# Kernel optimization log

Hardware: AMD Instinct MI355X
Metric: run time of the kernel (lower is better)

Reference implementation:

```python
import jax, jax.numpy as jnp
import numpy as np

N_PATCHES = 14
HIDDEN_D = 768
N_HEADS = 12
D_HEAD = HIDDEN_D // N_HEADS
OUT_D = 1000
IMG = 224
C = 3
PS = IMG // N_PATCHES  # 16
SEQ = N_PATCHES * N_PATCHES + 1  # 197
INPUT_D = C * PS * PS  # 768
EPS = 1e-5


def positional_embeddings(s, d):
    i = jnp.arange(s, dtype=jnp.float32)[:, None]
    j = jnp.arange(d, dtype=jnp.float32)[None, :]
    even = jnp.sin(i / jnp.power(10000.0, j / d))
    odd = jnp.cos(i / jnp.power(10000.0, (j - 1.0) / d))
    return jnp.where(jnp.arange(d)[None, :] % 2 == 0, even, odd)


def layernorm_2d(x, g, b):
    # torch nn.LayerNorm((S, D)): normalize over last two dims jointly, biased var
    mu = jnp.mean(x, axis=(-2, -1), keepdims=True)
    var = jnp.var(x, axis=(-2, -1), keepdims=True)
    return (x - mu) * jax.lax.rsqrt(var + EPS) * g + b


def setup_inputs() -> dict:
    key = jax.random.key(0)
    ks = jax.random.split(key, 16)
    s = 0.02
    return {
        "images": jax.random.normal(ks[0], (64, C, IMG, IMG), jnp.float32),
        "W_map": jax.random.normal(ks[1], (INPUT_D, HIDDEN_D), jnp.float32) * s,
        "b_map": jnp.zeros((HIDDEN_D,), jnp.float32),
        "cls_tok": jax.random.uniform(ks[2], (1, HIDDEN_D), jnp.float32),
        "ln1_g": jnp.ones((SEQ, HIDDEN_D), jnp.float32),
        "ln1_b": jnp.zeros((SEQ, HIDDEN_D), jnp.float32),
        "Wq": jax.random.normal(ks[3], (N_HEADS, D_HEAD, D_HEAD), jnp.float32) * s,
        "bq": jnp.zeros((N_HEADS, D_HEAD), jnp.float32),
        "Wk": jax.random.normal(ks[4], (N_HEADS, D_HEAD, D_HEAD), jnp.float32) * s,
        "bk": jnp.zeros((N_HEADS, D_HEAD), jnp.float32),
        "Wv": jax.random.normal(ks[5], (N_HEADS, D_HEAD, D_HEAD), jnp.float32) * s,
        "bv": jnp.zeros((N_HEADS, D_HEAD), jnp.float32),
        "ln2_g": jnp.ones((SEQ, HIDDEN_D), jnp.float32),
        "ln2_b": jnp.zeros((SEQ, HIDDEN_D), jnp.float32),
        "W_enc": jax.random.normal(ks[6], (HIDDEN_D, HIDDEN_D), jnp.float32) * s,
        "b_enc": jnp.zeros((HIDDEN_D,), jnp.float32),
        "W_out": jax.random.normal(ks[7], (HIDDEN_D, OUT_D), jnp.float32) * s,
        "b_out": jnp.zeros((OUT_D,), jnp.float32),
    }


def reference(images, W_map, b_map, cls_tok, ln1_g, ln1_b, Wq, bq, Wk, bk, Wv, bv,
              ln2_g, ln2_b, W_enc, b_enc, W_out, b_out):
    n = images.shape[0]
    # patchify: [N,C,H,W] -> [N, np*np, C*ps*ps], patch flattened in (C,ph,pw) order
    p = images.reshape(n, C, N_PATCHES, PS, N_PATCHES, PS)
    patches = p.transpose(0, 2, 4, 1, 3, 5).reshape(n, N_PATCHES * N_PATCHES, INPUT_D)

    tokens = patches @ W_map + b_map  # [N, np^2, D]
    cls = jnp.broadcast_to(cls_tok[None], (n, 1, HIDDEN_D))
    tokens = jnp.concatenate([cls, tokens], axis=1)  # [N, S, D]
    tokens = tokens + positional_embeddings(SEQ, HIDDEN_D)[None]

    # MSA on ln1(tokens), vectorized over batch and heads
    x = layernorm_2d(tokens, ln1_g, ln1_b)
    xh = x.reshape(n, SEQ, N_HEADS, D_HEAD)  # split hidden into heads
    q = jnp.einsum('bshd,hde->bshe', xh, Wq) + bq[None, None]
    k = jnp.einsum('bshd,hde->bshe', xh, Wk) + bk[None, None]
    v = jnp.einsum('bshd,hde->bshe', xh, Wv) + bv[None, None]
    scores = jnp.einsum('bshe,bthe->bhst', q, k) / np.sqrt(D_HEAD).astype(np.float32)
    attn = jax.nn.softmax(scores, axis=-1)  # [B,H,S,S]
    msa = jnp.einsum('bhst,bthe->bshe', attn, v).reshape(n, SEQ, HIDDEN_D)

    out = tokens + msa
    out = out + jax.nn.relu(layernorm_2d(out, ln2_g, ln2_b) @ W_enc + b_enc)
    cls_out = out[:, 0]  # [N, D]
    return jax.nn.softmax(cls_out @ W_out + b_out, axis=-1)
```

## Files before the change

kernel.cpp:

```cpp
#include <hip/hip_runtime.h>
#include <math.h>

#define SEQL 197
#define HD 768
#define NH 12
#define DHD 64
#define BATCH 64
#define OUTD 1000

typedef unsigned short ushort_t;
typedef __attribute__((ext_vector_type(8))) short bf16x8;
typedef __attribute__((ext_vector_type(4))) float f32x4;

static __device__ __forceinline__ unsigned short f2bf(float f) {
    union { float f; unsigned u; } v; v.f = f;
    unsigned r = v.u + 0x7fff + ((v.u >> 16) & 1);
    return (unsigned short)(r >> 16);
}

static __device__ __forceinline__ void gload16(const ushort_t* g, ushort_t* l) {
    __builtin_amdgcn_global_load_lds(
        (const __attribute__((address_space(1))) unsigned int*)g,
        (__attribute__((address_space(3))) unsigned int*)l, 16, 0, 0);
}

static __device__ __forceinline__ int xcd_chunk(int id, int nwg) {
    int xcd = id & 7, ii = id >> 3;
    int q = nwg >> 3, r = nwg & 7;
    return (xcd < r) ? (xcd * (q + 1) + ii) : (r * (q + 1) + (xcd - r) * q + ii);
}

#define NB_CVT  1296
#define NB_INIT 783
__global__ void k_prep(const float* __restrict__ W_map, const float* __restrict__ W_enc,
                       const float* __restrict__ Wq, const float* __restrict__ Wk,
                       const float* __restrict__ Wv, const float* __restrict__ cls_tok,
                       const float* __restrict__ img,
                       ushort_t* __restrict__ WmT, ushort_t* __restrict__ WeT,
                       ushort_t* __restrict__ wt, float* __restrict__ stats,
                       float* __restrict__ logits, float* __restrict__ pos,
                       float* __restrict__ tok, ushort_t* __restrict__ Ae) {
    const int bx = blockIdx.x, tid = threadIdx.x;
    if (bx < NB_CVT) {
        int idx = bx * 256 + tid;
        if (bx == 0) { stats[tid] = 0.f; }
        if (idx < BATCH * OUTD) logits[idx] = 0.f;
        if (idx < 2 * 147456) {
            const float* W = (idx < 147456) ? W_map : W_enc;
            ushort_t* WT   = (idx < 147456) ? WmT : WeT;
            int i = (idx < 147456) ? idx : idx - 147456;
            int k = i / 192, nq = i % 192;
            float4 w = *(const float4*)&W[k * 768 + nq * 4];
            WT[(nq * 4 + 0) * 768 + k] = f2bf(w.x);
            WT[(nq * 4 + 1) * 768 + k] = f2bf(w.y);
            WT[(nq * 4 + 2) * 768 + k] = f2bf(w.z);
            WT[(nq * 4 + 3) * 768 + k] = f2bf(w.w);
        } else {
            int i = idx - 2 * 147456;
            if (i < 36864) {
                int dq = i & 15;
                int e  = (i >> 4) & 63;
                int h  = (i >> 10) % 12;
                int pj = i / 12288;
                const float* W = (pj == 0) ? Wq : (pj == 1) ? Wk : Wv;
                ushort4 o;
                o.x = f2bf(W[(h * 64 + dq * 4 + 0) * 64 + e]);
                o.y = f2bf(W[(h * 64 + dq * 4 + 1) * 64 + e]);
                o.z = f2bf(W[(h * 64 + dq * 4 + 2) * 64 + e]);
                o.w = f2bf(W[(h * 64 + dq * 4 + 3) * 64 + e]);
                *(ushort4*)&wt[(size_t)((pj * 12 + h) * 64 + e) * 64 + dq * 4] = o;
            }
        }
    } else if (bx < NB_CVT + NB_INIT) {
        int i = (bx - NB_CVT) * 256 + tid;
        if (i < SEQL * HD) {
            int s = i / HD, d = i % HD;
            float f = (float)(d & ~1);
            float r = powf(10000.0f, -f / (float)HD);
            float a = (float)s * r;
            pos[i] = (d & 1) ? cosf(a) : sinf(a);
        } else {
            int j = i - SEQL * HD;
            int b = j / HD, e = j % HD;
            tok[(b * SEQL) * HD + e] = cls_tok[e] + ((e & 1) ? 1.0f : 0.0f);
        }
    } else if (bx == NB_CVT + NB_INIT) {
        __shared__ float rs[4], rs2[4];
        float s = 0.f, s2 = 0.f;
#pragma unroll
        for (int j = 0; j < 3; ++j) {
            int e = tid * 3 + j;
            float v = cls_tok[e] + ((e & 1) ? 1.0f : 0.0f);
            s += v; s2 += v * v;
        }
#pragma unroll
        for (int off = 32; off > 0; off >>= 1) {
            s += __shfl_down(s, off);
            s2 += __shfl_down(s2, off);
        }
        int lane = tid & 63, w = tid >> 6;
        if (lane == 0) { rs[w] = s; rs2[w] = s2; }
        __syncthreads();
        if (tid == 0) {
            float S = 0.f, S2 = 0.f;
#pragma unroll
            for (int i = 0; i < 4; ++i) { S += rs[i]; S2 += rs2[i]; }
            stats[256] = S;
            stats[257] = S2;
        }
    } else {
        int idx = (bx - (NB_CVT + NB_INIT + 1)) * 256 + tid;
        int m = idx / 192, kq = idx % 192;
        int k0 = kq * 4;
        int c = k0 >> 8, rem = k0 & 255, ir = rem >> 4, jc = rem & 15;
        int b = m / 196, pi = m % 196;
        int pr = pi / 14, pc = pi % 14;
        float4 v = *(const float4*)&img[((b * 3 + c) * 224 + pr * 16 + ir) * 224 + pc * 16 + jc];
        ushort4 o;
        o.x = f2bf(v.x); o.y = f2bf(v.y); o.z = f2bf(v.z); o.w = f2bf(v.w);
        *(ushort4*)&Ae[m * 768 + k0] = o;
    }
}

template <int MODE>
__launch_bounds__(256)
__global__ void k_gemm_bf16(const ushort_t* __restrict__ A, const ushort_t* __restrict__ Bt,
                            const float* __restrict__ bias, const float* __restrict__ pos,
                            float* __restrict__ out, int Mtot, float* __restrict__ stats,
                            int nwg) {
    __shared__ ushort_t As[2][128 * 64];
    __shared__ ushort_t Bs[2][128 * 64];
    __shared__ float redS[4][4];
    const int vid = xcd_chunk(blockIdx.x, nwg);
    const int m0 = (vid / 6) * 128;
    const int n0 = (vid % 6) * 128;
    const int tid = threadIdx.x;
    const int lane = tid & 63, wave = tid >> 6;
    const int wm = wave >> 1, wn = wave & 1;

    int stg_c[4], stg_row[4], stg_col[4];
#pragma unroll
    for (int t = 0; t < 4; ++t) {
        int c = (wave << 2) | t;
        int o = c * 1024 + lane * 16;
        int row = o >> 7;
        int inner = o & 127;
        stg_c[t] = c;
        stg_row[t] = row;
        stg_col[t] = (inner ^ ((row & 7) << 4)) >> 1;
    }

#define STAGE(BUF, K0)                                                                    \
    {                                                                                     \
        _Pragma("unroll") for (int t = 0; t < 4; ++t) {                                   \
            gload16(&A[(size_t)(m0 + stg_row[t]) * 768 + (K0) + stg_col[t]],              \
                    &As[BUF][stg_c[t] * 512]);                                            \
            gload16(&Bt[(size_t)(n0 + stg_row[t]) * 768 + (K0) + stg_col[t]],             \
                    &Bs[BUF][stg_c[t] * 512]);                                            \
        }                                                                                 \
    }

    f32x4 acc[4][4];
#pragma unroll
    for (int i = 0; i < 4; ++i)
#pragma unroll
        for (int j = 0; j < 4; ++j)
#pragma unroll
            for (int r = 0; r < 4; ++r) acc[i][j][r] = 0.f;

    STAGE(0, 0);
    __syncthreads();

    int cur = 0;
    for (int kt = 0; kt < 12; ++kt) {
        if (kt < 11) STAGE(cur ^ 1, (kt + 1) * 64);

#pragma unroll
        for (int ks = 0; ks < 2; ++ks) {
            const int cbyte = ks * 64 + (lane >> 4) * 16;
            bf16x8 af[4], bf[4];
#pragma unroll
            for (int mi = 0; mi < 4; ++mi) {
                int row = wm * 64 + mi * 16 + (lane & 15);
                af[mi] = *(const bf16x8*)((const char*)&As[cur][0] + row * 128 + (cbyte ^ ((row & 7) << 4)));
            }
#pragma unroll
            for (int ni = 0; ni < 4; ++ni) {
                int n = wn * 64 + ni * 16 + (lane & 15);
                bf[ni] = *(const bf16x8*)((const char*)&Bs[cur][0] + n * 128 + (cbyte ^ ((n & 7) << 4)));
            }
#pragma unroll
            for (int mi = 0; mi < 4; ++mi)
#pragma unroll
                for (int ni = 0; ni < 4; ++ni)
                    acc[mi][ni] = __builtin_amdgcn_mfma_f32_16x16x32_bf16(af[mi], bf[ni], acc[mi][ni], 0, 0, 0);
        }
        __syncthreads();
        cur ^= 1;
    }
#undef STAGE

    const int colb = n0 + wn * 64 + (lane & 15);
    const int rowb = m0 + wm * 64 + (lane >> 4) * 4;
    float s_lo = 0.f, q_lo = 0.f, s_hi = 0.f, q_hi = 0.f;
    const int bA = m0 / 196;
    const int mSplit = (bA + 1) * 196;
#pragma unroll
    for (int ni = 0; ni < 4; ++ni) {
        const int n = colb + ni * 16;
        const float bn = bias[n];
#pragma unroll
        for (int mi = 0; mi < 4; ++mi) {
#pragma unroll
            for (int r = 0; r < 4; ++r) {
                int m = rowb + mi * 16 + r;
                if (MODE == 0) {
                    int b = m / 196, s = 1 + m % 196;
                    float oval = acc[mi][ni][r] + bn + pos[s * HD + n];
                    out[((b * SEQL) + s) * HD + n] = oval;
                    if (m < mSplit) { s_lo += oval; q_lo += oval * oval; }
                    else            { s_hi += oval; q_hi += oval * oval; }
                } else {
                    if (m < Mtot) {
                        float* p = &out[(size_t)m * HD + n];
                        *p = *p + fmaxf(acc[mi][ni][r] + bn, 0.f);
                    }
                }
            }
        }
    }
    if (MODE == 0) {
#pragma unroll
        for (int off = 32; off > 0; off >>= 1) {
            s_lo += __shfl_down(s_lo, off);
            q_lo += __shfl_down(q_lo, off);
            s_hi += __shfl_down(s_hi, off);
            q_hi += __shfl_down(q_hi, off);
        }
        if (lane == 0) {
            redS[wave][0] = s_lo; redS[wave][1] = q_lo;
            redS[wave][2] = s_hi; redS[wave][3] = q_hi;
        }
        __syncthreads();
        if (tid == 0) {
            float a0 = 0.f, a1 = 0.f, a2 = 0.f, a3 = 0.f;
#pragma unroll
            for (int i = 0; i < 4; ++i) {
                a0 += redS[i][0]; a1 += redS[i][1];
                a2 += redS[i][2]; a3 += redS[i][3];
            }
            atomicAdd(&stats[2 * bA], a0);
            atomicAdd(&stats[2 * bA + 1], a1);
            int bB = bA + 1;
            if (bB < BATCH) {
                atomicAdd(&stats[2 * bB], a2);
                atomicAdd(&stats[2 * bB + 1], a3);
            }
        }
    }
}

__launch_bounds__(512, 2)
__global__ void k_qkvattn(const float* __restrict__ tok, float* __restrict__ stats,
                          const float* __restrict__ g1, const float* __restrict__ b1,
                          const ushort_t* __restrict__ wt,
                          const float* __restrict__ bq, const float* __restrict__ bk,
                          const float* __restrict__ bv, float* __restrict__ out) {
    const int h = blockIdx.x, b = blockIdx.y;
    __shared__ __attribute__((aligned(16))) ushort_t sm[32768];
    __shared__ float rS[8], rS2[8];
    const int tid = threadIdx.x;
    const int wave = tid >> 6, lane = tid & 63;
    const int l16 = lane & 15, l4 = lane >> 4;
    const int r0 = wave * 32;
    const float inv_n = 1.0f / (float)(SEQL * HD);
    const float S1_ = stats[b * 2] + stats[256];
    const float S2_ = stats[b * 2 + 1] + stats[257];
    const float mu = S1_ * inv_n;
    const float rsg = rsqrtf(S2_ * inv_n - mu * mu + 1e-5f);
    ushort_t* A16 = sm;
    ushort_t* B16 = sm + 16384;

    {
        const int row = tid >> 1, hw = tid & 1;
        if (row < SEQL) {
            const float* tp = &tok[((size_t)b * SEQL + row) * HD + h * 64 + hw * 32];
            const float* gp = &g1[(size_t)row * HD + h * 64 + hw * 32];
            const float* bp = &b1[(size_t)row * HD + h * 64 + hw * 32];
#pragma unroll
            for (int g = 0; g < 4; ++g) {
                float4 t0 = *(const float4*)&tp[g * 8];
                float4 t1 = *(const float4*)&tp[g * 8 + 4];
                float4 ga = *(const float4*)&gp[g * 8];
                float4 gb = *(const float4*)&gp[g * 8 + 4];
                float4 ba = *(const float4*)&bp[g * 8];
                float4 bb = *(const float4*)&bp[g * 8 + 4];
                bf16x8 o;
                o[0] = (short)f2bf((t0.x - mu) * rsg * ga.x + ba.x);
                o[1] = (short)f2bf((t0.y - mu) * rsg * ga.y + ba.y);
                o[2] = (short)f2bf((t0.z - mu) * rsg * ga.z + ba.z);
                o[3] = (short)f2bf((t0.w - mu) * rsg * ga.w + ba.w);
                o[4] = (short)f2bf((t1.x - mu) * rsg * gb.x + bb.x);
                o[5] = (short)f2bf((t1.y - mu) * rsg * gb.y + bb.y);
                o[6] = (short)f2bf((t1.z - mu) * rsg * gb.z + bb.z);
                o[7] = (short)f2bf((t1.w - mu) * rsg * gb.w + bb.w);
                int pc = (hw * 32 + g * 8) ^ ((row & 7) << 3);
                *(bf16x8*)&A16[row * 64 + pc] = o;
            }
        } else {
            bf16x8 z;
#pragma unroll
            for (int j = 0; j < 8; ++j) z[j] = 0;
#pragma unroll
            for (int g = 0; g < 4; ++g) {
                int pc = (hw * 32 + g * 8) ^ ((row & 7) << 3);
                *(bf16x8*)&A16[row * 64 + pc] = z;
            }
        }
    }

    bf16x8 af[2][2];
#pragma unroll
    for (int mi = 0; mi < 2; ++mi)
#pragma unroll
        for (int kk = 0; kk < 2; ++kk) {
            int row = r0 + mi * 16 + l16;
            af[mi][kk] = *(const bf16x8*)&A16[row * 64 + ((kk * 32 + l4 * 8) ^ ((row & 7) << 3))];
        }

#define PROJ_ACC(PJ, ACC)                                                                      \
    {                                                                                          \
        _Pragma("unroll") for (int ni = 0; ni < 4; ++ni) {                                     \
            const ushort_t* wr = &wt[(size_t)(((PJ) * 12 + h) * 64 + ni * 16 + l16) * 64];     \
            bf16x8 w0 = *(const bf16x8*)&wr[l4 * 8];                                           \
            bf16x8 w1 = *(const bf16x8*)&wr[32 + l4 * 8];                                      \
            _Pragma("unroll") for (int mi = 0; mi < 2; ++mi) {                                 \
                ACC[mi][ni] = __builtin_amdgcn_mfma_f32_16x16x32_bf16(af[mi][0], w0, ACC[mi][ni], 0, 0, 0); \
                ACC[mi][ni] = __builtin_amdgcn_mfma_f32_16x16x32_bf16(af[mi][1], w1, ACC[mi][ni], 0, 0, 0); \
            }                                                                                  \
        }                                                                                      \
    }

    f32x4 acc[2][4];
#define ZERO_ACC                                                                               \
    _Pragma("unroll") for (int mi = 0; mi < 2; ++mi)                                           \
        _Pragma("unroll") for (int ni = 0; ni < 4; ++ni) {                                     \
            acc[mi][ni][0] = 0.f; acc[mi][ni][1] = 0.f; acc[mi][ni][2] = 0.f; acc[mi][ni][3] = 0.f; }

    ZERO_ACC;
    PROJ_ACC(0, acc);
#pragma unroll
    for (int ni = 0; ni < 4; ++ni) {
        float bn = bq[h * 64 + ni * 16 + l16];
#pragma unroll
        for (int mi = 0; mi < 2; ++mi)
#pragma unroll
            for (int r = 0; r < 4; ++r) {
                int row = r0 + mi * 16 + l4 * 4 + r;
                A16[row * 64 + ((ni * 16 + l16) ^ ((row & 7) << 3))] = f2bf(acc[mi][ni][r] + bn);
            }
    }
    bf16x8 qa[2][2];
#pragma unroll
    for (int mi = 0; mi < 2; ++mi)
#pragma unroll
        for (int kk = 0; kk < 2; ++kk) {
            int row = r0 + mi * 16 + l16;
            qa[mi][kk] = *(const bf16x8*)&A16[row * 64 + ((kk * 32 + l4 * 8) ^ ((row & 7) << 3))];
        }

    ZERO_ACC;
    PROJ_ACC(1, acc);
#pragma unroll
    for (int ni = 0; ni < 4; ++ni) {
        float bn = bk[h * 64 + ni * 16 + l16];
#pragma unroll
        for (int mi = 0; mi < 2; ++mi)
#pragma unroll
            for (int r = 0; r < 4; ++r) {
                int t = r0 + mi * 16 + l4 * 4 + r;
                A16[t * 64 + ((ni * 16 + l16) ^ ((t & 7) << 3))] = f2bf(acc[mi][ni][r] + bn);
            }
    }

    ZERO_ACC;
    PROJ_ACC(2, acc);
#pragma unroll
    for (int ni = 0; ni < 4; ++ni) {
        float bn = bv[h * 64 + ni * 16 + l16];
#pragma unroll
        for (int mi = 0; mi < 2; ++mi) {
            int t4 = r0 + mi * 16 + l4 * 4;
            int e = ni * 16 + l16;
            ushort4 pkt;
            pkt.x = f2bf(acc[mi][ni][0] + bn);
            pkt.y = f2bf(acc[mi][ni][1] + bn);
            pkt.z = f2bf(acc[mi][ni][2] + bn);
            pkt.w = f2bf(acc[mi][ni][3] + bn);
            *(ushort4*)&B16[e * 256 + (t4 ^ ((e & 7) << 3))] = pkt;
        }
    }

    __syncthreads();

    f32x4 sa[2][16];
#pragma unroll
    for (int ni = 0; ni < 16; ++ni) {
        int t = ni * 16 + l16;
        bf16x8 k0 = *(const bf16x8*)&A16[t * 64 + ((l4 * 8) ^ ((t & 7) << 3))];
        bf16x8 k1 = *(const bf16x8*)&A16[t * 64 + ((32 + l4 * 8) ^ ((t & 7) << 3))];
#pragma unroll
        for (int mi = 0; mi < 2; ++mi) {
            f32x4 z;
            z[0] = 0.f; z[1] = 0.f; z[2] = 0.f; z[3] = 0.f;
            z = __builtin_amdgcn_mfma_f32_16x16x32_bf16(qa[mi][0], k0, z, 0, 0, 0);
            sa[mi][ni] = __builtin_amdgcn_mfma_f32_16x16x32_bf16(qa[mi][1], k1, z, 0, 0, 0);
        }
    }

    float l_s[2][4];
#pragma unroll
    for (int mi = 0; mi < 2; ++mi)
#pragma unroll
        for (int r = 0; r < 4; ++r) {
            float rsum = 0.f;
#pragma unroll
            for (int ni = 0; ni < 16; ++ni) {
                float p = (ni * 16 + l16 < SEQL) ? __expf(sa[mi][ni][r] * 0.125f) : 0.f;
                sa[mi][ni][r] = p;
                rsum += p;
            }
            rsum += __shfl_xor(rsum, 1);
            rsum += __shfl_xor(rsum, 2);
            rsum += __shfl_xor(rsum, 4);
            rsum += __shfl_xor(rsum, 8);
            l_s[mi][r] = rsum;
        }

    __syncthreads();

    f32x4 oacc[2][4];
#pragma unroll
    for (int mi = 0; mi < 2; ++mi)
#pragma unroll
        for (int ne = 0; ne < 4; ++ne) {
            oacc[mi][ne][0] = 0.f; oacc[mi][ne][1] = 0.f;
            oacc[mi][ne][2] = 0.f; oacc[mi][ne][3] = 0.f;
        }

    for (int c = 0; c < 4; ++c) {
#pragma unroll
        for (int j = 0; j < 4; ++j)
#pragma unroll
            for (int mi = 0; mi < 2; ++mi)
#pragma unroll
                for (int r = 0; r < 4; ++r) {
                    int row = r0 + mi * 16 + l4 * 4 + r;
                    A16[row * 64 + ((j * 16 + l16) ^ ((row & 7) << 3))] = f2bf(sa[mi][c * 4 + j][r]);
                }
        bf16x8 pa[2][2];
#pragma unroll
        for (int mi = 0; mi < 2; ++mi)
#pragma unroll
            for (int kk = 0; kk < 2; ++kk) {
                int row = r0 + mi * 16 + l16;
                pa[mi][kk] = *(const bf16x8*)&A16[row * 64 + ((kk * 32 + l4 * 8) ^ ((row & 7) << 3))];
            }
#pragma unroll
        for (int ne = 0; ne < 4; ++ne) {
            int e = ne * 16 + l16;
            bf16x8 v0 = *(const bf16x8*)&B16[e * 256 + ((c * 64 + l4 * 8) ^ ((e & 7) << 3))];
            bf16x8 v1 = *(const bf16x8*)&B16[e * 256 + ((c * 64 + 32 + l4 * 8) ^ ((e & 7) << 3))];
#pragma unroll
            for (int mi = 0; mi < 2; ++mi) {
                oacc[mi][ne] = __builtin_amdgcn_mfma_f32_16x16x32_bf16(pa[mi][0], v0, oacc[mi][ne], 0, 0, 0);
                oacc[mi][ne] = __builtin_amdgcn_mfma_f32_16x16x32_bf16(pa[mi][1], v1, oacc[mi][ne], 0, 0, 0);
            }
        }
    }

    __syncthreads();
    float* Osm = (float*)sm + wave * 2048;
#pragma unroll
    for (int mi = 0; mi < 2; ++mi)
#pragma unroll
        for (int r = 0; r < 4; ++r) {
            float inv = 1.0f / l_s[mi][r];
            int rl = mi * 16 + l4 * 4 + r;
#pragma unroll
            for (int ne = 0; ne < 4; ++ne)
                Osm[rl * 64 + ((ne * 16 + l16) ^ ((rl & 3) << 4))] = oacc[mi][ne][r] * inv;
        }
    float psum = 0.f, psq = 0.f;
#pragma unroll
    for (int it = 0; it < 8; ++it) {
        int rl = it * 4 + l4;
        int row = r0 + rl;
        if (row < SEQL) {
            size_t off = ((size_t)b * SEQL + row) * HD + h * 64 + l16 * 4;
            float4 ov = *(float4*)&Osm[rl * 64 + ((l16 * 4) ^ ((rl & 3) << 4))];
            float4 tv = *(const float4*)&tok[off];
            float4 o;
            o.x = ov.x + tv.x; o.y = ov.y + tv.y;
            o.z = ov.z + tv.z; o.w = ov.w + tv.w;
            *(float4*)&out[off] = o;
            psum += o.x + o.y + o.z + o.w;
            psq  += o.x * o.x + o.y * o.y + o.z * o.z + o.w * o.w;
        }
    }
#pragma unroll
    for (int off = 32; off > 0; off >>= 1) {
        psum += __shfl_down(psum, off);
        psq += __shfl_down(psq, off);
    }
    if (lane == 0) { rS[wave] = psum; rS2[wave] = psq; }
    __syncthreads();
    if (tid == 0) {
        float S = 0.f, S2 = 0.f;
#pragma unroll
        for (int i = 0; i < 8; ++i) { S += rS[i]; S2 += rS2[i]; }
        atomicAdd(&stats[128 + 2 * b], S);
        atomicAdd(&stats[129 + 2 * b], S2);
    }
#undef PROJ_ACC
#undef ZERO_ACC
}

__global__ void k_ln2apply(const float* __restrict__ outb, const float* __restrict__ stats,
                           const float* __restrict__ g2, const float* __restrict__ b2,
                           ushort_t* __restrict__ x) {
    int i = blockIdx.x * 256 + threadIdx.x;
    if (i >= BATCH * SEQL * HD / 4) return;
    int e4 = i * 4;
    int m = e4 / HD, kk = e4 % HD;
    int b = m / SEQL, s = m % SEQL;
    const float inv_n = 1.0f / (float)(SEQL * HD);
    float S = stats[128 + 2 * b], S2 = stats[129 + 2 * b];
    float mu = S * inv_n;
    float rsg = rsqrtf(S2 * inv_n - mu * mu + 1e-5f);
    float4 t = *(const float4*)&outb[e4];
    float4 g = *(const float4*)&g2[s * HD + kk];
    float4 bb = *(const float4*)&b2[s * HD + kk];
    ushort4 o;
    o.x = f2bf((t.x - mu) * rsg * g.x + bb.x);
    o.y = f2bf((t.y - mu) * rsg * g.y + bb.y);
    o.z = f2bf((t.z - mu) * rsg * g.z + bb.z);
    o.w = f2bf((t.w - mu) * rsg * g.w + bb.w);
    *(ushort4*)&x[e4] = o;
}

__launch_bounds__(256)
__global__ void k_logits(const float* __restrict__ out, const float* __restrict__ Wo,
                         float* __restrict__ logits) {
    const int eg = blockIdx.x, b = blockIdx.y, tid = threadIdx.x;
    __shared__ float cls[192];
    if (tid < 48)
        *(float4*)&cls[tid * 4] = *(const float4*)&out[(size_t)(b * SEQL) * HD + eg * 192 + tid * 4];
    __syncthreads();
    const int o0 = tid * 4;
    if (o0 < OUTD) {
        float4 acc = {0.f, 0.f, 0.f, 0.f};
        const float* wbase = &Wo[(size_t)eg * 192 * OUTD + o0];
#pragma unroll 4
        for (int e = 0; e < 192; ++e) {
            float c = cls[e];
            float4 w = *(const float4*)&wbase[(size_t)e * OUTD];
            acc.x += c * w.x;
            acc.y += c * w.y;
            acc.z += c * w.z;
            acc.w += c * w.w;
        }
        atomicAdd(&logits[b * OUTD + o0 + 0], acc.x);
        atomicAdd(&logits[b * OUTD + o0 + 1], acc.y);
        atomicAdd(&logits[b * OUTD + o0 + 2], acc.z);
        atomicAdd(&logits[b * OUTD + o0 + 3], acc.w);
    }
}

__launch_bounds__(256)
__global__ void k_head_sm(const float* __restrict__ logits, const float* __restrict__ bo,
                          float* __restrict__ dout) {
    const int b = blockIdx.x, tid = threadIdx.x;
    __shared__ float red[256];
    const int o0 = tid * 4;
    const bool ok = (o0 < OUTD);
    float4 acc = {0.f, 0.f, 0.f, 0.f};
    if (ok) {
        float4 lg = *(const float4*)&logits[b * OUTD + o0];
        float4 bb = *(const float4*)&bo[o0];
        acc.x = lg.x + bb.x; acc.y = lg.y + bb.y;
        acc.z = lg.z + bb.z; acc.w = lg.w + bb.w;
    }
    float mx = ok ? fmaxf(fmaxf(acc.x, acc.y), fmaxf(acc.z, acc.w)) : -INFINITY;
    red[tid] = mx;
    __syncthreads();
    for (int s = 128; s > 0; s >>= 1) {
        if (tid < s) red[tid] = fmaxf(red[tid], red[tid + s]);
        __syncthreads();
    }
    float M = red[0];
    __syncthreads();
    float4 p = {0.f, 0.f, 0.f, 0.f};
    float ls = 0.f;
    if (ok) {
        p.x = expf(acc.x - M);
        p.y = expf(acc.y - M);
        p.z = expf(acc.z - M);
        p.w = expf(acc.w - M);
        ls = p.x + p.y + p.z + p.w;
    }
    red[tid] = ls;
    __syncthreads();
    for (int s = 128; s > 0; s >>= 1) {
        if (tid < s) red[tid] += red[tid + s];
        __syncthreads();
    }
    float inv = 1.0f / red[0];
    if (ok) {
        p.x *= inv; p.y *= inv; p.z *= inv; p.w *= inv;
        *(float4*)&dout[b * OUTD + o0] = p;
    }
}

extern "C" void kernel_launch(void* const* d_in, const int* in_sizes, int n_in,
                              void* d_out, int out_size, void* d_ws, size_t ws_size,
                              hipStream_t stream) {
    const float* images  = (const float*)d_in[0];
    const float* W_map   = (const float*)d_in[1];
    const float* b_map   = (const float*)d_in[2];
    const float* cls_tok = (const float*)d_in[3];
    const float* ln1_g   = (const float*)d_in[4];
    const float* ln1_b   = (const float*)d_in[5];
    const float* Wq      = (const float*)d_in[6];
    const float* bq      = (const float*)d_in[7];
    const float* Wk      = (const float*)d_in[8];
    const float* bk      = (const float*)d_in[9];
    const float* Wv      = (const float*)d_in[10];
    const float* bv      = (const float*)d_in[11];
    const float* ln2_g   = (const float*)d_in[12];
    const float* ln2_b   = (const float*)d_in[13];
    const float* W_enc   = (const float*)d_in[14];
    const float* b_enc   = (const float*)d_in[15];
    const float* W_out   = (const float*)d_in[16];
    const float* b_out   = (const float*)d_in[17];

    float* ws = (float*)d_ws;
    const size_t BIG = (size_t)BATCH * SEQL * HD;

    float* pos   = ws;
    float* tok   = ws + 151552;
    float* outb  = tok + BIG;
    float* stats = outb + BIG;
    ushort_t* wtq = (ushort_t*)(stats + 512);
    ushort_t* Ae  = wtq + 147456;
    ushort_t* WmT = Ae + (size_t)12672 * 768;
    ushort_t* WeT = WmT + (size_t)768 * 768;
    float* logits = (float*)(WeT + (size_t)768 * 768);
    ushort_t* Ae2 = Ae;

    k_prep<<<11488, 256, 0, stream>>>(W_map, W_enc, Wq, Wk, Wv, cls_tok, images,
                                      WmT, WeT, wtq, stats, logits, pos, tok, Ae);
    k_gemm_bf16<0><<<588, 256, 0, stream>>>(Ae, WmT, b_map, pos, tok, 12544, stats, 588);
    k_qkvattn<<<dim3(12, 64), 512, 0, stream>>>(tok, stats, ln1_g, ln1_b, wtq, bq, bk, bv, outb);
    k_ln2apply<<<9456, 256, 0, stream>>>(outb, stats, ln2_g, ln2_b, Ae2);
    k_gemm_bf16<1><<<594, 256, 0, stream>>>(Ae2, WeT, b_enc, pos, outb, 12608, stats, 594);
    k_logits<<<dim3(4, 64), 256, 0, stream>>>(outb, W_out, logits);
    k_head_sm<<<64, 256, 0, stream>>>(logits, b_out, (float*)d_out);
}
```

Baseline: 233.5 us.

## Stream attention through per-wave P tiles to cut registers and raise occupancy

```diff
diff --git a/kernel.cpp b/kernel.cpp
--- a/kernel.cpp
+++ b/kernel.cpp
@@ -260,15 +260,14 @@
     }
 }
 
-__launch_bounds__(512, 2)
+__launch_bounds__(512, 4)
 __global__ void k_qkvattn(const float* __restrict__ tok, float* __restrict__ stats,
                           const float* __restrict__ g1, const float* __restrict__ b1,
                           const ushort_t* __restrict__ wt,
                           const float* __restrict__ bq, const float* __restrict__ bk,
                           const float* __restrict__ bv, float* __restrict__ out) {
     const int h = blockIdx.x, b = blockIdx.y;
-    __shared__ __attribute__((aligned(16))) ushort_t sm[32768];
-    __shared__ float rS[8], rS2[8];
+    __shared__ __attribute__((aligned(16))) ushort_t sm[37888];
     const int tid = threadIdx.x;
     const int wave = tid >> 6, lane = tid & 63;
     const int l16 = lane & 15, l4 = lane >> 4;
@@ -280,6 +279,7 @@
     const float rsg = rsqrtf(S2_ * inv_n - mu * mu + 1e-5f);
     ushort_t* A16 = sm;
     ushort_t* B16 = sm + 16384;
+    ushort_t* Pw  = sm + 32768 + wave * 640;
 
     {
         const int row = tid >> 1, hw = tid & 1;
@@ -403,93 +403,80 @@
 
     __syncthreads();
 
-    f32x4 sa[2][16];
-#pragma unroll
-    for (int ni = 0; ni < 16; ++ni) {
-        int t = ni * 16 + l16;
-        bf16x8 k0 = *(const bf16x8*)&A16[t * 64 + ((l4 * 8) ^ ((t & 7) << 3))];
-        bf16x8 k1 = *(const bf16x8*)&A16[t * 64 + ((32 + l4 * 8) ^ ((t & 7) << 3))];
-#pragma unroll
-        for (int mi = 0; mi < 2; ++mi) {
-            f32x4 z;
-            z[0] = 0.f; z[1] = 0.f; z[2] = 0.f; z[3] = 0.f;
-            z = __builtin_amdgcn_mfma_f32_16x16x32_bf16(qa[mi][0], k0, z, 0, 0, 0);
-            sa[mi][ni] = __builtin_amdgcn_mfma_f32_16x16x32_bf16(qa[mi][1], k1, z, 0, 0, 0);
+    f32x4 oacc[2][4];
+#pragma unroll
+    for (int p = 0; p < 2; ++p)
+#pragma unroll
+        for (int ne = 0; ne < 4; ++ne) {
+            oacc[p][ne][0] = 0.f; oacc[p][ne][1] = 0.f;
+            oacc[p][ne][2] = 0.f; oacc[p][ne][3] = 0.f;
+        }
+    float rsum[2][4];
+#pragma unroll
+    for (int p = 0; p < 2; ++p)
+#pragma unroll
+        for (int r = 0; r < 4; ++r) rsum[p][r] = 0.f;
+
+#pragma unroll
+    for (int p = 0; p < 2; ++p) {
+        for (int c = 0; c < 8; ++c) {
+            const int t0 = c * 32 + l16;
+            const int t1 = t0 + 16;
+            bf16x8 k00 = *(const bf16x8*)&A16[t0 * 64 + ((l4 * 8) ^ ((t0 & 7) << 3))];
+            bf16x8 k01 = *(const bf16x8*)&A16[t0 * 64 + ((32 + l4 * 8) ^ ((t0 & 7) << 3))];
+            bf16x8 k10 = *(const bf16x8*)&A16[t1 * 64 + ((l4 * 8) ^ ((t1 & 7) << 3))];
+            bf16x8 k11 = *(const bf16x8*)&A16[t1 * 64 + ((32 + l4 * 8) ^ ((t1 & 7) << 3))];
+            f32x4 z0, z1;
+            z0[0] = 0.f; z0[1] = 0.f; z0[2] = 0.f; z0[3] = 0.f;
+            z1[0] = 0.f; z1[1] = 0.f; z1[2] = 0.f; z1[3] = 0.f;
+            z0 = __builtin_amdgcn_mfma_f32_16x16x32_bf16(qa[p][0], k00, z0, 0, 0, 0);
+            z0 = __builtin_amdgcn_mfma_f32_16x16x32_bf16(qa[p][1], k01, z0, 0, 0, 0);
+            z1 = __builtin_amdgcn_mfma_f32_16x16x32_bf16(qa[p][0], k10, z1, 0, 0, 0);
+            z1 = __builtin_amdgcn_mfma_f32_16x16x32_bf16(qa[p][1], k11, z1, 0, 0, 0);
+            const bool ok0 = (t0 < SEQL), ok1 = (t1 < SEQL);
+#pragma unroll
+            for (int r = 0; r < 4; ++r) {
+                float p0 = ok0 ? __expf(z0[r] * 0.125f) : 0.f;
+                float p1 = ok1 ? __expf(z1[r] * 0.125f) : 0.f;
+                rsum[p][r] += p0 + p1;
+                int ql = l4 * 4 + r;
+                Pw[ql * 40 + l16] = f2bf(p0);
+                Pw[ql * 40 + 16 + l16] = f2bf(p1);
+            }
+            bf16x8 pa = *(const bf16x8*)&Pw[l16 * 40 + l4 * 8];
+#pragma unroll
+            for (int ne = 0; ne < 4; ++ne) {
+                int e = ne * 16 + l16;
+                bf16x8 vv = *(const bf16x8*)&B16[e * 256 + ((c * 32 + l4 * 8) ^ ((e & 7) << 3))];
+                oacc[p][ne] = __builtin_amdgcn_mfma_f32_16x16x32_bf16(pa, vv, oacc[p][ne], 0, 0, 0);
+            }
         }
     }
 
     float l_s[2][4];
 #pragma unroll
-    for (int mi = 0; mi < 2; ++mi)
+    for (int p = 0; p < 2; ++p)
 #pragma unroll
         for (int r = 0; r < 4; ++r) {
-            float rsum = 0.f;
-#pragma unroll
-            for (int ni = 0; ni < 16; ++ni) {
-                float p = (ni * 16 + l16 < SEQL) ? __expf(sa[mi][ni][r] * 0.125f) : 0.f;
-                sa[mi][ni][r] = p;
-                rsum += p;
-            }
-            rsum += __shfl_xor(rsum, 1);
-            rsum += __shfl_xor(rsum, 2);
-            rsum += __shfl_xor(rsum, 4);
-            rsum += __shfl_xor(rsum, 8);
-            l_s[mi][r] = rsum;
-        }
-
-    __syncthreads();
-
-    f32x4 oacc[2][4];
-#pragma unroll
-    for (int mi = 0; mi < 2; ++mi)
-#pragma unroll
-        for (int ne = 0; ne < 4; ++ne) {
-            oacc[mi][ne][0] = 0.f; oacc[mi][ne][1] = 0.f;
-            oacc[mi][ne][2] = 0.f; oacc[mi][ne][3] = 0.f;
-        }
-
-    for (int c = 0; c < 4; ++c) {
-#pragma unroll
-        for (int j = 0; j < 4; ++j)
-#pragma unroll
-            for (int mi = 0; mi < 2; ++mi)
-#pragma unroll
-                for (int r = 0; r < 4; ++r) {
-                    int row = r0 + mi * 16 + l4 * 4 + r;
-                    A16[row * 64 + ((j * 16 + l16) ^ ((row & 7) << 3))] = f2bf(sa[mi][c * 4 + j][r]);
-                }
-        bf16x8 pa[2][2];
-#pragma unroll
-        for (int mi = 0; mi < 2; ++mi)
-#pragma unroll
-            for (int kk = 0; kk < 2; ++kk) {
-                int row = r0 + mi * 16 + l16;
-                pa[mi][kk] = *(const bf16x8*)&A16[row * 64 + ((kk * 32 + l4 * 8) ^ ((row & 7) << 3))];
-            }
-#pragma unroll
-        for (int ne = 0; ne < 4; ++ne) {
-            int e = ne * 16 + l16;
-            bf16x8 v0 = *(const bf16x8*)&B16[e * 256 + ((c * 64 + l4 * 8) ^ ((e & 7) << 3))];
-            bf16x8 v1 = *(const bf16x8*)&B16[e * 256 + ((c * 64 + 32 + l4 * 8) ^ ((e & 7) << 3))];
-#pragma unroll
-            for (int mi = 0; mi < 2; ++mi) {
-                oacc[mi][ne] = __builtin_amdgcn_mfma_f32_16x16x32_bf16(pa[mi][0], v0, oacc[mi][ne], 0, 0, 0);
-                oacc[mi][ne] = __builtin_amdgcn_mfma_f32_16x16x32_bf16(pa[mi][1], v1, oacc[mi][ne], 0, 0, 0);
-            }
-        }
-    }
+            float rs = rsum[p][r];
+            rs += __shfl_xor(rs, 1);
+            rs += __shfl_xor(rs, 2);
+            rs += __shfl_xor(rs, 4);
+            rs += __shfl_xor(rs, 8);
+            l_s[p][r] = rs;
+        }
 
     __syncthreads();
     float* Osm = (float*)sm + wave * 2048;
 #pragma unroll
-    for (int mi = 0; mi < 2; ++mi)
+    for (int p = 0; p < 2; ++p)
 #pragma unroll
         for (int r = 0; r < 4; ++r) {
-            float inv = 1.0f / l_s[mi][r];
-            int rl = mi * 16 + l4 * 4 + r;
+            float inv = 1.0f / l_s[p][r];
+            int rl = p * 16 + l4 * 4 + r;
 #pragma unroll
             for (int ne = 0; ne < 4; ++ne)
-                Osm[rl * 64 + ((ne * 16 + l16) ^ ((rl & 3) << 4))] = oacc[mi][ne][r] * inv;
+                Osm[rl * 64 + ((ne * 16 + l16) ^ ((rl & 3) << 4))] = oacc[p][ne][r] * inv;
         }
     float psum = 0.f, psq = 0.f;
 #pragma unroll
@@ -513,14 +500,9 @@
         psum += __shfl_down(psum, off);
         psq += __shfl_down(psq, off);
     }
-    if (lane == 0) { rS[wave] = psum; rS2[wave] = psq; }
-    __syncthreads();
-    if (tid == 0) {
-        float S = 0.f, S2 = 0.f;
-#pragma unroll
-        for (int i = 0; i < 8; ++i) { S += rS[i]; S2 += rS2[i]; }
-        atomicAdd(&stats[128 + 2 * b], S);
-        atomicAdd(&stats[129 + 2 * b], S2);
+    if (lane == 0) {
+        atomicAdd(&stats[128 + 2 * b], psum);
+        atomicAdd(&stats[129 + 2 * b], psq);
     }
 #undef PROJ_ACC
 #undef ZERO_ACC
```

New measurement: 261.6 us. 1.12x slower.
